# Performance work log

Measured on AMD Instinct MI355X. Metric: run time of the kernel, lower is better.

## Reference

```python
import jax, jax.numpy as jnp
import numpy as np

HEADS = 16

def setup_inputs() -> dict:
    key = jax.random.key(0)
    ks = jax.random.split(key, 8)
    B, Lq, G, Lkv, dim, dim_kv = 4, 512, 4, 1024, 1024, 1024
    inner = dim_kv  # dim_per_head * heads = (dim_kv // heads) * heads
    H = jax.random.normal(ks[0], (B, Lq, dim), dtype=jnp.float32)
    KV = jax.random.normal(ks[1], (B, G, Lkv, dim_kv), dtype=jnp.float32)
    KV_mask = jax.random.randint(ks[2], (B, G, Lkv), 0, 2, dtype=jnp.int32)
    s = 0.02
    Wq = jax.random.normal(ks[3], (dim, inner), dtype=jnp.float32) * s
    Wk = jax.random.normal(ks[4], (dim_kv, inner), dtype=jnp.float32) * s
    Wv = jax.random.normal(ks[5], (dim_kv, inner), dtype=jnp.float32) * s
    Wo = jax.random.normal(ks[6], (inner, dim), dtype=jnp.float32) * s
    return {"H": H, "KV": KV, "KV_mask": KV_mask,
            "Wq": Wq, "Wk": Wk, "Wv": Wv, "Wo": Wo}


def reference(H, KV, KV_mask, Wq, Wk, Wv, Wo):
    B, Lq, dim = H.shape
    _, G, Lkv, dim_kv = KV.shape
    inner = Wq.shape[1]
    h = HEADS
    d = inner // h

    # q: [B, h, Lq, d], pre-scaled as in the torch module
    q = (H @ Wq).reshape(B, Lq, h, d).transpose(0, 2, 1, 3) * (d ** -0.5)
    # k, v: [B, G, h, Lkv, d] -- all graphs batched instead of Python loop
    k = jnp.einsum('bgle,ef->bglf', KV, Wk).reshape(B, G, Lkv, h, d).transpose(0, 1, 3, 2, 4)
    v = jnp.einsum('bgle,ef->bglf', KV, Wv).reshape(B, G, Lkv, h, d).transpose(0, 1, 3, 2, 4)

    # scores: [B, G, h, Lq, Lkv]
    scores = jnp.einsum('bhqd,bghkd->bghqk', q, k)
    # additive mask: (1 - mask) * finfo.min, mask broadcast over heads & queries
    mask = KV_mask.astype(scores.dtype)  # [B, G, Lkv]
    scores = scores + (1.0 - mask)[:, :, None, None, :] * jnp.finfo(scores.dtype).min

    attn = jax.nn.softmax(scores.astype(jnp.float32), axis=-1).astype(scores.dtype)
    ctx = jnp.einsum('bghqk,bghkd->bghqd', attn, v)  # [B, G, h, Lq, d]
    ctx = ctx.transpose(0, 1, 3, 2, 4).reshape(B, G, Lq, inner)
    out = ctx @ Wo  # [B, G, Lq, dim]
    # concat over graphs along last dim, matching torch.cat(all_attn, dim=-1)
    out = out.transpose(0, 2, 1, 3).reshape(B, Lq, G * dim)
    return out
```

## Files before the change

### kernel.cpp

```cpp
#include <hip/hip_runtime.h>

using f16   = _Float16;
using f16x8 = _Float16 __attribute__((ext_vector_type(8)));
using f16x4 = _Float16 __attribute__((ext_vector_type(4)));
using f32x4 = float    __attribute__((ext_vector_type(4)));

constexpr int BM = 128, BN = 128, BK = 64;
constexpr int KD = 1024, ND = 1024;

__device__ __forceinline__ int swz(int r, int c) {
  return r * BK + ((c ^ (r & 7)) << 3);
}

__device__ __forceinline__ void gload_lds16(const f16* g, f16* s) {
  __builtin_amdgcn_global_load_lds(
      (const __attribute__((address_space(1))) void*)g,
      (__attribute__((address_space(3))) void*)s, 16, 0, 0);
}

__global__ __launch_bounds__(256)
void cast_k(const float* __restrict__ in, f16* __restrict__ out) {
  size_t i = ((size_t)blockIdx.x * 256 + threadIdx.x) * 8;
  f32x4 a = *(const f32x4*)(in + i);
  f32x4 b = *(const f32x4*)(in + i + 4);
  f16x8 o;
  o[0] = (f16)a[0]; o[1] = (f16)a[1]; o[2] = (f16)a[2]; o[3] = (f16)a[3];
  o[4] = (f16)b[0]; o[5] = (f16)b[1]; o[6] = (f16)b[2]; o[7] = (f16)b[3];
  *(f16x8*)(out + i) = o;
}

__global__ __launch_bounds__(256)
void wtrans_k(const float* __restrict__ W, f16* __restrict__ Wt) {
  __shared__ float tile[32][33];
  int bx = blockIdx.x * 32;
  int by = blockIdx.y * 32;
  int tx = threadIdx.x, ty = threadIdx.y;
#pragma unroll
  for (int i = 0; i < 4; ++i) {
    int r = ty + i * 8;
    tile[r][tx] = W[(size_t)(by + r) * ND + bx + tx];
  }
  __syncthreads();
#pragma unroll
  for (int i = 0; i < 4; ++i) {
    int r = ty + i * 8;
    Wt[(size_t)(bx + r) * KD + by + tx] = (f16)tile[tx][r];
  }
}

template <int MODE>
__global__ __launch_bounds__(256)
void gemm_k(const f16* __restrict__ A, const f16* __restrict__ Bt,
            void* __restrict__ C, float scale) {
  __shared__ __attribute__((aligned(16))) f16 As[BM * BK];
  __shared__ __attribute__((aligned(16))) f16 Bs[BN * BK];
  const int t = threadIdx.x;
  const int w = t >> 6, l = t & 63, l15 = l & 15, lg = l >> 4;
  const int m0 = blockIdx.y * BM, n0 = blockIdx.x * BN;
  const int wm = (w >> 1) * 64, wn = (w & 1) * 64;
  const int lr  = l >> 3;
  const int csw = ((l & 7) ^ lr) << 3;

  const f16* Ab = A  + (size_t)m0 * KD + csw;
  const f16* Bb = Bt + (size_t)n0 * KD + csw;

  f32x4 acc[4][4] = {};

  for (int kb = 0; kb < KD; kb += BK) {
#pragma unroll
    for (int i = 0; i < 4; ++i) {
      int ii = w * 4 + i;
      int r  = ii * 8 + lr;
      gload_lds16(Ab + (size_t)r * KD + kb, &As[ii * 512]);
      gload_lds16(Bb + (size_t)r * KD + kb, &Bs[ii * 512]);
    }
    __syncthreads();
#pragma unroll
    for (int ks = 0; ks < 2; ++ks) {
      f16x8 av[4], bw[4];
      int cc = ks * 4 + lg;
#pragma unroll
      for (int mf = 0; mf < 4; ++mf)
        av[mf] = *(const f16x8*)&As[swz(wm + mf * 16 + l15, cc)];
#pragma unroll
      for (int nf = 0; nf < 4; ++nf)
        bw[nf] = *(const f16x8*)&Bs[swz(wn + nf * 16 + l15, cc)];
#pragma unroll
      for (int mf = 0; mf < 4; ++mf)
#pragma unroll
        for (int nf = 0; nf < 4; ++nf)
          acc[mf][nf] = __builtin_amdgcn_mfma_f32_16x16x32_f16(
              av[mf], bw[nf], acc[mf][nf], 0, 0, 0);
    }
    __syncthreads();
  }

#pragma unroll
  for (int mf = 0; mf < 4; ++mf) {
#pragma unroll
    for (int nf = 0; nf < 4; ++nf) {
      int mb = m0 + wm + mf * 16 + 4 * lg;
      int n  = n0 + wn + nf * 16 + l15;
      if (MODE == 0) {
#pragma unroll
        for (int r = 0; r < 4; ++r)
          ((f16*)C)[(size_t)(mb + r) * ND + n] = (f16)(acc[mf][nf][r] * scale);
      } else if (MODE == 1) {
        int bg = mb >> 10, kv = mb & 1023;
        int h = n >> 6, e = n & 63;
        f16x4 pk;
#pragma unroll
        for (int r = 0; r < 4; ++r) pk[r] = (f16)acc[mf][nf][r];
        *(f16x4*)((f16*)C + (size_t)((bg * 16 + h) * 64 + e) * 1024 + kv) = pk;
      } else {
#pragma unroll
        for (int r = 0; r < 4; ++r) {
          int m = mb + r;
          int bg = m >> 9, lq = m & 511;
          int bb = bg >> 2, g = bg & 3;
          ((float*)C)[(size_t)(((bb << 9) + lq) * 4 + g) * 1024 + n] =
              acc[mf][nf][r];
        }
      }
    }
  }
}

__global__ __launch_bounds__(256)
void attn_k(const f16* __restrict__ Qb, const f16* __restrict__ Kb,
            const f16* __restrict__ Vt, const int* __restrict__ mask,
            f16* __restrict__ ctx) {
  __shared__ int smask[1024];
  __shared__ __attribute__((aligned(16))) f16 Ks[64 * 64];
  __shared__ __attribute__((aligned(16))) f16 Vs[64 * 64];
  __shared__ __attribute__((aligned(16))) f16 Pl[4][32 * 72];

  const int t = threadIdx.x, w = t >> 6, l = t & 63, l15 = l & 15, lg = l >> 4;
  const int y = blockIdx.y, bg = y >> 4, h = y & 15, bb = bg >> 2;
  const int q0 = blockIdx.x * 128 + w * 32;
  const int lr = l >> 3, csw = ((l & 7) ^ lr) << 3;

  *(int4*)&smask[t * 4] = *(const int4*)(mask + bg * 1024 + t * 4);

  f16x8 aQ[2][2];
#pragma unroll
  for (int mf = 0; mf < 2; ++mf) {
    const f16* qp =
        Qb + (size_t)(bb * 512 + q0 + mf * 16 + l15) * 1024 + h * 64 + lg * 8;
    aQ[mf][0] = *(const f16x8*)qp;
    aQ[mf][1] = *(const f16x8*)(qp + 32);
  }

  float mrow[2][4], rs[2][4];
#pragma unroll
  for (int mf = 0; mf < 2; ++mf)
#pragma unroll
    for (int r = 0; r < 4; ++r) { mrow[mf][r] = -1e30f; rs[mf][r] = 0.f; }
  f32x4 accO[2][4] = {};

  const f16* Kbase = Kb + (size_t)bg * (1024 * 1024) + h * 64 + csw;
  const f16* Vbase = Vt + (size_t)(bg * 16 + h) * (64 * 1024) + csw;

  __syncthreads();

  for (int c16 = 0; c16 < 16; ++c16) {
    const int kv0 = c16 * 64;
#pragma unroll
    for (int i = 0; i < 2; ++i) {
      int ii = w * 2 + i;
      int r  = ii * 8 + lr;
      gload_lds16(Kbase + (size_t)(kv0 + r) * 1024, &Ks[ii * 512]);
      gload_lds16(Vbase + (size_t)r * 1024 + kv0,   &Vs[ii * 512]);
    }
    __syncthreads();

    f32x4 s[2][4] = {};
#pragma unroll
    for (int nf = 0; nf < 4; ++nf) {
      int kr = nf * 16 + l15;
      f16x8 k0 = *(const f16x8*)&Ks[swz(kr, lg)];
      f16x8 k1 = *(const f16x8*)&Ks[swz(kr, 4 + lg)];
#pragma unroll
      for (int mf = 0; mf < 2; ++mf) {
        s[mf][nf] = __builtin_amdgcn_mfma_f32_16x16x32_f16(aQ[mf][0], k0, s[mf][nf], 0, 0, 0);
        s[mf][nf] = __builtin_amdgcn_mfma_f32_16x16x32_f16(aQ[mf][1], k1, s[mf][nf], 0, 0, 0);
      }
    }
#pragma unroll
    for (int nf = 0; nf < 4; ++nf) {
      if (smask[kv0 + nf * 16 + l15] == 0) {
#pragma unroll
        for (int mf = 0; mf < 2; ++mf)
#pragma unroll
          for (int r = 0; r < 4; ++r) s[mf][nf][r] = -1e30f;
      }
    }
#pragma unroll
    for (int mf = 0; mf < 2; ++mf)
#pragma unroll
      for (int r = 0; r < 4; ++r) {
        float v = fmaxf(fmaxf(s[mf][0][r], s[mf][1][r]),
                        fmaxf(s[mf][2][r], s[mf][3][r]));
        v = fmaxf(v, __shfl_xor(v, 1));
        v = fmaxf(v, __shfl_xor(v, 2));
        v = fmaxf(v, __shfl_xor(v, 4));
        v = fmaxf(v, __shfl_xor(v, 8));
        float mn = fmaxf(mrow[mf][r], v);
        float sc = __expf(mrow[mf][r] - mn);
        mrow[mf][r] = mn;
        rs[mf][r] *= sc;
#pragma unroll
        for (int nf = 0; nf < 4; ++nf) accO[mf][nf][r] *= sc;
        float ps = 0.f;
#pragma unroll
        for (int nf = 0; nf < 4; ++nf) {
          float p = __expf(s[mf][nf][r] - mn);
          ps += p;
          Pl[w][(mf * 16 + 4 * lg + r) * 72 + nf * 16 + l15] = (f16)p;
        }
        rs[mf][r] += ps;
      }
#pragma unroll
    for (int ks = 0; ks < 2; ++ks) {
      f16x8 aP[2];
#pragma unroll
      for (int mf = 0; mf < 2; ++mf)
        aP[mf] = *(const f16x8*)&Pl[w][(mf * 16 + l15) * 72 + ks * 32 + lg * 8];
#pragma unroll
      for (int nf = 0; nf < 4; ++nf) {
        f16x8 bV = *(const f16x8*)&Vs[swz(nf * 16 + l15, ks * 4 + lg)];
#pragma unroll
        for (int mf = 0; mf < 2; ++mf)
          accO[mf][nf] = __builtin_amdgcn_mfma_f32_16x16x32_f16(aP[mf], bV, accO[mf][nf], 0, 0, 0);
      }
    }
    __syncthreads();
  }

#pragma unroll
  for (int mf = 0; mf < 2; ++mf)
#pragma unroll
    for (int r = 0; r < 4; ++r) {
      float v = rs[mf][r];
      v += __shfl_xor(v, 1);
      v += __shfl_xor(v, 2);
      v += __shfl_xor(v, 4);
      v += __shfl_xor(v, 8);
      rs[mf][r] = 1.0f / v;
    }
#pragma unroll
  for (int mf = 0; mf < 2; ++mf)
#pragma unroll
    for (int nf = 0; nf < 4; ++nf)
#pragma unroll
      for (int r = 0; r < 4; ++r) {
        int q = q0 + mf * 16 + 4 * lg + r;
        ctx[(size_t)(bg * 512 + q) * 1024 + h * 64 + nf * 16 + l15] =
            (f16)(accO[mf][nf][r] * rs[mf][r]);
      }
}

extern "C" void kernel_launch(void* const* d_in, const int* in_sizes, int n_in,
                              void* d_out, int out_size, void* d_ws,
                              size_t ws_size, hipStream_t stream) {
  const float* H  = (const float*)d_in[0];
  const float* KV = (const float*)d_in[1];
  const int*  msk = (const int*)d_in[2];
  const float* Wq = (const float*)d_in[3];
  const float* Wk = (const float*)d_in[4];
  const float* Wv = (const float*)d_in[5];
  const float* Wo = (const float*)d_in[6];

  char* ws = (char*)d_ws;
  f16* WqT  = (f16*)(ws + ((size_t)0  << 20));
  f16* WkT  = (f16*)(ws + ((size_t)2  << 20));
  f16* WvT  = (f16*)(ws + ((size_t)4  << 20));
  f16* WoT  = (f16*)(ws + ((size_t)6  << 20));
  f16* Hf   = (f16*)(ws + ((size_t)8  << 20));
  f16* KVf  = (f16*)(ws + ((size_t)12 << 20));
  f16* Qb   = (f16*)(ws + ((size_t)12 << 20));
  f16* ctxf = (f16*)(ws + ((size_t)16 << 20));
  f16* Kb   = (f16*)(ws + ((size_t)44 << 20));
  f16* Vtb  = (f16*)(ws + ((size_t)76 << 20));

  cast_k<<<1024, 256, 0, stream>>>(H,  Hf);
  cast_k<<<8192, 256, 0, stream>>>(KV, KVf);

  dim3 tb32(32, 8);
  wtrans_k<<<dim3(32, 32), tb32, 0, stream>>>(Wq, WqT);
  wtrans_k<<<dim3(32, 32), tb32, 0, stream>>>(Wk, WkT);
  wtrans_k<<<dim3(32, 32), tb32, 0, stream>>>(Wv, WvT);
  wtrans_k<<<dim3(32, 32), tb32, 0, stream>>>(Wo, WoT);

  gemm_k<0><<<dim3(8, 128), 256, 0, stream>>>(KVf, WkT, (void*)Kb,  1.0f);
  gemm_k<1><<<dim3(8, 128), 256, 0, stream>>>(KVf, WvT, (void*)Vtb, 1.0f);
  gemm_k<0><<<dim3(8, 16),  256, 0, stream>>>(Hf,  WqT, (void*)Qb,  0.125f);

  attn_k<<<dim3(4, 256), 256, 0, stream>>>(Qb, Kb, Vtb, msk, ctxf);

  gemm_k<2><<<dim3(8, 64), 256, 0, stream>>>(ctxf, WoT, d_out, 1.0f);
}
```

Measured before the change: 403.9 us.

## Double-buffer attention K/V tiles, lazy softmax rescale, XCD-swizzled GEMM grid

Several ideas at once. The attention kernel now double-buffers the K/V LDS tiles, prefetching the next tile while computing the current one under explicit vmcnt waits. It hoists the V fragment loads, halves the P scratch buffer by processing one row fragment at a time, and raises wave priority around the MFMA blocks. It also skips the online-softmax rescale unless the running max grows by more than 8, and the GEMM kernel remaps block indices so neighbouring tiles land on the same XCD. The lazy rescale allows unnormalised exponentials up to e^8 in fp16 P, and the single P buffer per wave relies on correct intra-wave ordering.

```diff
diff --git a/kernel.cpp b/kernel.cpp
--- a/kernel.cpp
+++ b/kernel.cpp
@@ -16,6 +16,13 @@
   __builtin_amdgcn_global_load_lds(
       (const __attribute__((address_space(1))) void*)g,
       (__attribute__((address_space(3))) void*)s, 16, 0, 0);
+}
+
+__device__ __forceinline__ int2 xcd_swz() {
+  int lin = blockIdx.y * gridDim.x + blockIdx.x;
+  int per = (gridDim.x * gridDim.y) >> 3;
+  int sw  = (lin & 7) * per + (lin >> 3);
+  return make_int2(sw % gridDim.x, sw / gridDim.x);
 }
 
 __global__ __launch_bounds__(256)
@@ -56,7 +63,8 @@
   __shared__ __attribute__((aligned(16))) f16 Bs[BN * BK];
   const int t = threadIdx.x;
   const int w = t >> 6, l = t & 63, l15 = l & 15, lg = l >> 4;
-  const int m0 = blockIdx.y * BM, n0 = blockIdx.x * BN;
+  const int2 bi = xcd_swz();
+  const int m0 = bi.y * BM, n0 = bi.x * BN;
   const int wm = (w >> 1) * 64, wn = (w & 1) * 64;
   const int lr  = l >> 3;
   const int csw = ((l & 7) ^ lr) << 3;
@@ -131,9 +139,9 @@
             const f16* __restrict__ Vt, const int* __restrict__ mask,
             f16* __restrict__ ctx) {
   __shared__ int smask[1024];
-  __shared__ __attribute__((aligned(16))) f16 Ks[64 * 64];
-  __shared__ __attribute__((aligned(16))) f16 Vs[64 * 64];
-  __shared__ __attribute__((aligned(16))) f16 Pl[4][32 * 72];
+  __shared__ __attribute__((aligned(16))) f16 Ks[2][64 * 64];
+  __shared__ __attribute__((aligned(16))) f16 Vs[2][64 * 64];
+  __shared__ __attribute__((aligned(16))) f16 Pl[4][16 * 72];
 
   const int t = threadIdx.x, w = t >> 6, l = t & 63, l15 = l & 15, lg = l >> 4;
   const int y = blockIdx.y, bg = y >> 4, h = y & 15, bb = bg >> 2;
@@ -161,31 +169,46 @@
   const f16* Kbase = Kb + (size_t)bg * (1024 * 1024) + h * 64 + csw;
   const f16* Vbase = Vt + (size_t)(bg * 16 + h) * (64 * 1024) + csw;
 
-  __syncthreads();
-
-  for (int c16 = 0; c16 < 16; ++c16) {
-    const int kv0 = c16 * 64;
+  auto stage = [&](int tile, int buf) {
+    const int kv0 = tile * 64;
 #pragma unroll
     for (int i = 0; i < 2; ++i) {
       int ii = w * 2 + i;
       int r  = ii * 8 + lr;
-      gload_lds16(Kbase + (size_t)(kv0 + r) * 1024, &Ks[ii * 512]);
-      gload_lds16(Vbase + (size_t)r * 1024 + kv0,   &Vs[ii * 512]);
-    }
-    __syncthreads();
+      gload_lds16(Kbase + (size_t)(kv0 + r) * 1024, &Ks[buf][ii * 512]);
+      gload_lds16(Vbase + (size_t)r * 1024 + kv0,   &Vs[buf][ii * 512]);
+    }
+  };
+
+  __syncthreads();
+  stage(0, 0);
+
+  for (int c16 = 0; c16 < 16; ++c16) {
+    const int cur = c16 & 1;
+    const int kv0 = c16 * 64;
+    if (c16 < 15) {
+      stage(c16 + 1, cur ^ 1);
+      asm volatile("s_waitcnt vmcnt(4)" ::: "memory");
+    } else {
+      asm volatile("s_waitcnt vmcnt(0)" ::: "memory");
+    }
+    __builtin_amdgcn_s_barrier();
+    __builtin_amdgcn_sched_barrier(0);
 
     f32x4 s[2][4] = {};
+    __builtin_amdgcn_s_setprio(1);
 #pragma unroll
     for (int nf = 0; nf < 4; ++nf) {
       int kr = nf * 16 + l15;
-      f16x8 k0 = *(const f16x8*)&Ks[swz(kr, lg)];
-      f16x8 k1 = *(const f16x8*)&Ks[swz(kr, 4 + lg)];
+      f16x8 k0 = *(const f16x8*)&Ks[cur][swz(kr, lg)];
+      f16x8 k1 = *(const f16x8*)&Ks[cur][swz(kr, 4 + lg)];
 #pragma unroll
       for (int mf = 0; mf < 2; ++mf) {
         s[mf][nf] = __builtin_amdgcn_mfma_f32_16x16x32_f16(aQ[mf][0], k0, s[mf][nf], 0, 0, 0);
         s[mf][nf] = __builtin_amdgcn_mfma_f32_16x16x32_f16(aQ[mf][1], k1, s[mf][nf], 0, 0, 0);
       }
     }
+    __builtin_amdgcn_s_setprio(0);
 #pragma unroll
     for (int nf = 0; nf < 4; ++nf) {
       if (smask[kv0 + nf * 16 + l15] == 0) {
@@ -195,8 +218,15 @@
           for (int r = 0; r < 4; ++r) s[mf][nf][r] = -1e30f;
       }
     }
-#pragma unroll
-    for (int mf = 0; mf < 2; ++mf)
+    f16x8 bV[2][4];
+#pragma unroll
+    for (int ks = 0; ks < 2; ++ks)
+#pragma unroll
+      for (int nf = 0; nf < 4; ++nf)
+        bV[ks][nf] = *(const f16x8*)&Vs[cur][swz(nf * 16 + l15, ks * 4 + lg)];
+
+#pragma unroll
+    for (int mf = 0; mf < 2; ++mf) {
 #pragma unroll
       for (int r = 0; r < 4; ++r) {
         float v = fmaxf(fmaxf(s[mf][0][r], s[mf][1][r]),
@@ -205,36 +235,36 @@
         v = fmaxf(v, __shfl_xor(v, 2));
         v = fmaxf(v, __shfl_xor(v, 4));
         v = fmaxf(v, __shfl_xor(v, 8));
-        float mn = fmaxf(mrow[mf][r], v);
-        float sc = __expf(mrow[mf][r] - mn);
-        mrow[mf][r] = mn;
-        rs[mf][r] *= sc;
-#pragma unroll
-        for (int nf = 0; nf < 4; ++nf) accO[mf][nf][r] *= sc;
+        float mn = mrow[mf][r];
+        if (v > mn + 8.f) {
+          float sc = __expf(mn - v);
+          mn = v; mrow[mf][r] = v;
+          rs[mf][r] *= sc;
+#pragma unroll
+          for (int nf = 0; nf < 4; ++nf) accO[mf][nf][r] *= sc;
+        }
         float ps = 0.f;
 #pragma unroll
         for (int nf = 0; nf < 4; ++nf) {
           float p = __expf(s[mf][nf][r] - mn);
           ps += p;
-          Pl[w][(mf * 16 + 4 * lg + r) * 72 + nf * 16 + l15] = (f16)p;
+          Pl[w][(4 * lg + r) * 72 + nf * 16 + l15] = (f16)p;
         }
         rs[mf][r] += ps;
       }
-#pragma unroll
-    for (int ks = 0; ks < 2; ++ks) {
-      f16x8 aP[2];
-#pragma unroll
-      for (int mf = 0; mf < 2; ++mf)
-        aP[mf] = *(const f16x8*)&Pl[w][(mf * 16 + l15) * 72 + ks * 32 + lg * 8];
-#pragma unroll
-      for (int nf = 0; nf < 4; ++nf) {
-        f16x8 bV = *(const f16x8*)&Vs[swz(nf * 16 + l15, ks * 4 + lg)];
-#pragma unroll
-        for (int mf = 0; mf < 2; ++mf)
-          accO[mf][nf] = __builtin_amdgcn_mfma_f32_16x16x32_f16(aP[mf], bV, accO[mf][nf], 0, 0, 0);
-      }
-    }
-    __syncthreads();
+      __builtin_amdgcn_s_setprio(1);
+#pragma unroll
+      for (int ks = 0; ks < 2; ++ks) {
+        f16x8 aP = *(const f16x8*)&Pl[w][l15 * 72 + ks * 32 + lg * 8];
+#pragma unroll
+        for (int nf = 0; nf < 4; ++nf)
+          accO[mf][nf] = __builtin_amdgcn_mfma_f32_16x16x32_f16(aP, bV[ks][nf], accO[mf][nf], 0, 0, 0);
+      }
+      __builtin_amdgcn_s_setprio(0);
+    }
+
+    asm volatile("s_waitcnt lgkmcnt(0)" ::: "memory");
+    __builtin_amdgcn_s_barrier();
   }
 
 #pragma unroll
```

Result: faster. 386.2 us (-4.4%).
